# Optimization experiments

Hardware: AMD Instinct MI355X
Metric: run time of the kernel (lower is better)

## Reference

```python
import jax, jax.numpy as jnp
import numpy as np

N_NODES = 4096
N_EDGES = 100000
N_PAIRS = 1000000
MAX_PATH = 5
EDGE_DIM = 16


def setup_inputs() -> dict:
    key = jax.random.key(0)
    k1, k2, k3, k4, k5, k6 = jax.random.split(key, 6)
    x = jax.random.normal(k1, (N_NODES, EDGE_DIM), dtype=jnp.float32)
    edge_attr = jax.random.normal(k2, (N_EDGES, EDGE_DIM), dtype=jnp.float32)
    edge_vector = jax.random.normal(k3, (MAX_PATH, EDGE_DIM), dtype=jnp.float32)
    # unique (src, dst) pairs so the scatter-set is well-defined (matches the
    # dict-of-dicts edge_paths, where each (src, dst) appears at most once)
    pair_ids = jax.random.permutation(k4, N_NODES * N_NODES)[:N_PAIRS]
    src_idx = (pair_ids // N_NODES).astype(jnp.int64)
    dst_idx = (pair_ids % N_NODES).astype(jnp.int64)
    # ragged paths: random length in [1, MAX_PATH], padded with -1
    path_idx = jax.random.randint(k5, (N_PAIRS, MAX_PATH), 0, N_EDGES).astype(jnp.int64)
    lengths = jax.random.randint(k6, (N_PAIRS, 1), 1, MAX_PATH + 1)
    valid = jnp.arange(MAX_PATH)[None, :] < lengths
    path_idx = jnp.where(valid, path_idx, -1)
    return {"x": x, "edge_attr": edge_attr, "edge_vector": edge_vector,
            "src_idx": src_idx, "dst_idx": dst_idx, "path_idx": path_idx}


def reference(x, edge_attr, edge_vector, src_idx, dst_idx, path_idx):
    # path_idx: [P, L] edge indices, -1 = padding beyond the path length
    n = x.shape[0]
    mask = path_idx >= 0                                   # [P, L]
    safe = jnp.where(mask, path_idx, 0)
    feats = edge_attr[safe]                                # [P, L, D] irregular gather
    dots = jnp.einsum('pld,ld->pl', feats, edge_vector)    # per-hop dot products
    dots = jnp.where(mask, dots, 0.0)
    cnt = mask.sum(axis=-1)                                # path lengths
    # mean over the path; empty path -> 0 (matches nan_to_num on 0/0)
    vals = jnp.where(cnt > 0, dots.sum(axis=-1) / jnp.maximum(cnt, 1).astype(dots.dtype), 0.0)
    cij = jnp.zeros((n, n), dtype=x.dtype).at[src_idx, dst_idx].set(vals)
    return cij
```

## Files before the change

kernel.cpp:

```cpp
#include <hip/hip_runtime.h>

#define N_NODES  4096
#define MAX_PATH 5
#define EDGE_DIM 16

__global__ __launch_bounds__(256) void precompute_dots_kernel(
    const float* __restrict__ edge_attr,
    const float* __restrict__ edge_vector,
    float*       __restrict__ D,
    int n_edges)
{
    int e = blockIdx.x * blockDim.x + threadIdx.x;
    if (e >= n_edges) return;

    const float4* ea = (const float4*)(edge_attr + (size_t)e * EDGE_DIM);
    float4 a0 = ea[0], a1 = ea[1], a2 = ea[2], a3 = ea[3];

#pragma unroll
    for (int l = 0; l < MAX_PATH; ++l) {
        const float4* ev = (const float4*)(edge_vector + l * EDGE_DIM);
        float4 b0 = ev[0], b1 = ev[1], b2 = ev[2], b3 = ev[3];
        float d = a0.x*b0.x + a0.y*b0.y + a0.z*b0.z + a0.w*b0.w
                + a1.x*b1.x + a1.y*b1.y + a1.z*b1.z + a1.w*b1.w
                + a2.x*b2.x + a2.y*b2.y + a2.z*b2.z + a2.w*b2.w
                + a3.x*b3.x + a3.y*b3.y + a3.z*b3.z + a3.w*b3.w;
        D[(size_t)l * n_edges + e] = d;
    }
}

__global__ __launch_bounds__(256) void edge_encoding_kernel(
    const float* __restrict__ D,
    const int*   __restrict__ src_idx,
    const int*   __restrict__ dst_idx,
    const int*   __restrict__ path_idx,
    float*       __restrict__ out,
    int n_pairs, int n_edges)
{
    int t  = blockIdx.x * blockDim.x + threadIdx.x;
    int p0 = t * 4;
    if (p0 >= n_pairs) return;

    if (p0 + 3 < n_pairs) {
        const int4* pp = (const int4*)(path_idx + (size_t)p0 * MAX_PATH);
        int4 w0 = pp[0], w1 = pp[1], w2 = pp[2], w3 = pp[3], w4 = pp[4];
        int e[20] = { w0.x, w0.y, w0.z, w0.w,
                      w1.x, w1.y, w1.z, w1.w,
                      w2.x, w2.y, w2.z, w2.w,
                      w3.x, w3.y, w3.z, w3.w,
                      w4.x, w4.y, w4.z, w4.w };

        float g[20];
#pragma unroll
        for (int j = 0; j < 4; ++j) {
#pragma unroll
            for (int l = 0; l < MAX_PATH; ++l) {
                int idx = e[j * MAX_PATH + l];
                g[j * MAX_PATH + l] = (idx >= 0) ? D[(size_t)l * n_edges + idx] : 0.0f;
            }
        }

        int4 sv = *(const int4*)(src_idx + p0);
        int4 dv = *(const int4*)(dst_idx + p0);
        int srcs[4] = { sv.x, sv.y, sv.z, sv.w };
        int dsts[4] = { dv.x, dv.y, dv.z, dv.w };

#pragma unroll
        for (int j = 0; j < 4; ++j) {
            float sum = 0.0f;
            int   cnt = 0;
#pragma unroll
            for (int l = 0; l < MAX_PATH; ++l) {
                int idx = e[j * MAX_PATH + l];
                if (idx >= 0) { sum += g[j * MAX_PATH + l]; ++cnt; }
            }
            float val = (cnt > 0) ? (sum / (float)cnt) : 0.0f;
            out[(size_t)srcs[j] * N_NODES + dsts[j]] = val;
        }
    } else {
        for (int p = p0; p < n_pairs; ++p) {
            float sum = 0.0f;
            int   cnt = 0;
#pragma unroll
            for (int l = 0; l < MAX_PATH; ++l) {
                int idx = path_idx[(size_t)p * MAX_PATH + l];
                if (idx >= 0) { sum += D[(size_t)l * n_edges + idx]; ++cnt; }
            }
            float val = (cnt > 0) ? (sum / (float)cnt) : 0.0f;
            out[(size_t)src_idx[p] * N_NODES + dst_idx[p]] = val;
        }
    }
}

extern "C" void kernel_launch(void* const* d_in, const int* in_sizes, int n_in,
                              void* d_out, int out_size, void* d_ws, size_t ws_size,
                              hipStream_t stream)
{
    const float* edge_attr   = (const float*)d_in[1];
    const float* edge_vector = (const float*)d_in[2];
    const int*   src_idx     = (const int*)d_in[3];
    const int*   dst_idx     = (const int*)d_in[4];
    const int*   path_idx    = (const int*)d_in[5];
    float*       out         = (float*)d_out;
    float*       D           = (float*)d_ws;

    const int n_edges = in_sizes[1] / EDGE_DIM;
    const int n_pairs = in_sizes[3];

    hipMemsetAsync(d_out, 0, (size_t)out_size * sizeof(float), stream);

    const int block = 256;
    precompute_dots_kernel<<<(n_edges + block - 1) / block, block, 0, stream>>>(
        edge_attr, edge_vector, D, n_edges);

    const int threads_needed = (n_pairs + 3) / 4;
    edge_encoding_kernel<<<(threads_needed + block - 1) / block, block, 0, stream>>>(
        D, src_idx, dst_idx, path_idx, out, n_pairs, n_edges);
}
```

Before: 47.17 us.

## Store precomputed dots in fp16, use 2 pairs per thread and nontemporal access

The precomputed per-edge dot table is stored as half precision, halving its footprint (2MB to 1MB) so the random gathers hit cache more often. Each thread now handles 2 pairs instead of 4, which doubles the thread count and uses 8-byte vector loads. Loads of the streaming indices and the scattered output stores become nontemporal. Rounding the dots to fp16 adds error, which may exceed the tolerance.

```diff
diff --git a/kernel.cpp b/kernel.cpp
--- a/kernel.cpp
+++ b/kernel.cpp
@@ -1,13 +1,16 @@
 #include <hip/hip_runtime.h>
+#include <hip/hip_fp16.h>
 
 #define N_NODES  4096
 #define MAX_PATH 5
 #define EDGE_DIM 16
 
+typedef int iv2 __attribute__((ext_vector_type(2)));
+
 __global__ __launch_bounds__(256) void precompute_dots_kernel(
     const float* __restrict__ edge_attr,
     const float* __restrict__ edge_vector,
-    float*       __restrict__ D,
+    __half*      __restrict__ D,
     int n_edges)
 {
     int e = blockIdx.x * blockDim.x + threadIdx.x;
@@ -24,57 +27,58 @@
                 + a1.x*b1.x + a1.y*b1.y + a1.z*b1.z + a1.w*b1.w
                 + a2.x*b2.x + a2.y*b2.y + a2.z*b2.z + a2.w*b2.w
                 + a3.x*b3.x + a3.y*b3.y + a3.z*b3.z + a3.w*b3.w;
-        D[(size_t)l * n_edges + e] = d;
+        D[(size_t)l * n_edges + e] = __float2half(d);
     }
 }
 
 __global__ __launch_bounds__(256) void edge_encoding_kernel(
-    const float* __restrict__ D,
-    const int*   __restrict__ src_idx,
-    const int*   __restrict__ dst_idx,
-    const int*   __restrict__ path_idx,
-    float*       __restrict__ out,
+    const __half* __restrict__ D,
+    const int*    __restrict__ src_idx,
+    const int*    __restrict__ dst_idx,
+    const int*    __restrict__ path_idx,
+    float*        __restrict__ out,
     int n_pairs, int n_edges)
 {
     int t  = blockIdx.x * blockDim.x + threadIdx.x;
-    int p0 = t * 4;
+    int p0 = t * 2;
     if (p0 >= n_pairs) return;
 
-    if (p0 + 3 < n_pairs) {
-        const int4* pp = (const int4*)(path_idx + (size_t)p0 * MAX_PATH);
-        int4 w0 = pp[0], w1 = pp[1], w2 = pp[2], w3 = pp[3], w4 = pp[4];
-        int e[20] = { w0.x, w0.y, w0.z, w0.w,
-                      w1.x, w1.y, w1.z, w1.w,
-                      w2.x, w2.y, w2.z, w2.w,
-                      w3.x, w3.y, w3.z, w3.w,
-                      w4.x, w4.y, w4.z, w4.w };
+    if (p0 + 1 < n_pairs) {
+        const iv2* pp = (const iv2*)(path_idx + (size_t)p0 * MAX_PATH);
+        iv2 w0 = __builtin_nontemporal_load(pp + 0);
+        iv2 w1 = __builtin_nontemporal_load(pp + 1);
+        iv2 w2 = __builtin_nontemporal_load(pp + 2);
+        iv2 w3 = __builtin_nontemporal_load(pp + 3);
+        iv2 w4 = __builtin_nontemporal_load(pp + 4);
+        int e[10] = { w0.x, w0.y, w1.x, w1.y, w2.x,
+                      w2.y, w3.x, w3.y, w4.x, w4.y };
 
-        float g[20];
+        float g[10];
 #pragma unroll
-        for (int j = 0; j < 4; ++j) {
+        for (int j = 0; j < 2; ++j) {
 #pragma unroll
             for (int l = 0; l < MAX_PATH; ++l) {
                 int idx = e[j * MAX_PATH + l];
-                g[j * MAX_PATH + l] = (idx >= 0) ? D[(size_t)l * n_edges + idx] : 0.0f;
+                g[j * MAX_PATH + l] =
+                    (idx >= 0) ? __half2float(D[(size_t)l * n_edges + idx]) : 0.0f;
             }
         }
 
-        int4 sv = *(const int4*)(src_idx + p0);
-        int4 dv = *(const int4*)(dst_idx + p0);
-        int srcs[4] = { sv.x, sv.y, sv.z, sv.w };
-        int dsts[4] = { dv.x, dv.y, dv.z, dv.w };
+        iv2 sv = __builtin_nontemporal_load((const iv2*)(src_idx + p0));
+        iv2 dv = __builtin_nontemporal_load((const iv2*)(dst_idx + p0));
+        int srcs[2] = { sv.x, sv.y };
+        int dsts[2] = { dv.x, dv.y };
 
 #pragma unroll
-        for (int j = 0; j < 4; ++j) {
+        for (int j = 0; j < 2; ++j) {
             float sum = 0.0f;
             int   cnt = 0;
 #pragma unroll
             for (int l = 0; l < MAX_PATH; ++l) {
-                int idx = e[j * MAX_PATH + l];
-                if (idx >= 0) { sum += g[j * MAX_PATH + l]; ++cnt; }
+                if (e[j * MAX_PATH + l] >= 0) { sum += g[j * MAX_PATH + l]; ++cnt; }
             }
             float val = (cnt > 0) ? (sum / (float)cnt) : 0.0f;
-            out[(size_t)srcs[j] * N_NODES + dsts[j]] = val;
+            __builtin_nontemporal_store(val, out + (size_t)srcs[j] * N_NODES + dsts[j]);
         }
     } else {
         for (int p = p0; p < n_pairs; ++p) {
@@ -83,10 +87,10 @@
 #pragma unroll
             for (int l = 0; l < MAX_PATH; ++l) {
                 int idx = path_idx[(size_t)p * MAX_PATH + l];
-                if (idx >= 0) { sum += D[(size_t)l * n_edges + idx]; ++cnt; }
+                if (idx >= 0) { sum += __half2float(D[(size_t)l * n_edges + idx]); ++cnt; }
             }
             float val = (cnt > 0) ? (sum / (float)cnt) : 0.0f;
-            out[(size_t)src_idx[p] * N_NODES + dst_idx[p]] = val;
+            __builtin_nontemporal_store(val, out + (size_t)src_idx[p] * N_NODES + dst_idx[p]);
         }
     }
 }
@@ -101,7 +105,7 @@
     const int*   dst_idx     = (const int*)d_in[4];
     const int*   path_idx    = (const int*)d_in[5];
     float*       out         = (float*)d_out;
-    float*       D           = (float*)d_ws;
+    __half*      D           = (__half*)d_ws;
 
     const int n_edges = in_sizes[1] / EDGE_DIM;
     const int n_pairs = in_sizes[3];
@@ -112,7 +116,7 @@
     precompute_dots_kernel<<<(n_edges + block - 1) / block, block, 0, stream>>>(
         edge_attr, edge_vector, D, n_edges);
 
-    const int threads_needed = (n_pairs + 3) / 4;
+    const int threads_needed = (n_pairs + 1) / 2;
     edge_encoding_kernel<<<(threads_needed + block - 1) / block, block, 0, stream>>>(
         D, src_idx, dst_idx, path_idx, out, n_pairs, n_edges);
 }
```

Result: slower. 68.34 us (+44.9%).
